# Performance work log

Measured on AMD Instinct MI355X. Metric: run time of the kernel, lower is better.

The kernel has to match this reference:

```python
import jax, jax.numpy as jnp
import numpy as np

TAU = 0.07
EPS = 1e-10


def setup_inputs() -> dict:
    key = jax.random.key(0)
    k1, k2 = jax.random.split(key)
    N, D = 8192, 128
    features = jax.random.normal(k1, (N, D), dtype=jnp.float32)
    alpha = jnp.float32(0.5)  # cosine-similarity threshold in (-1, 1)
    return {"features": features, "alpha": alpha}


def reference(features, alpha):
    # L2-normalize rows (torch F.normalize uses eps=1e-12 clamp on the norm)
    norm = jnp.maximum(jnp.linalg.norm(features, axis=1, keepdims=True), 1e-12)
    f = features / norm
    sim = f @ f.T  # [N, N]

    n = f.shape[0]
    not_eye = ~jnp.eye(n, dtype=bool)
    pos_mask = (sim >= alpha) & not_eye
    neg_mask = (sim < alpha) & not_eye

    e = jnp.exp(sim / TAU)  # [N, N], computed once and reused for both masks
    numerator = jnp.sum(jnp.where(pos_mask, e, 0.0), axis=1) + EPS
    denominator = numerator + jnp.sum(jnp.where(neg_mask, e, 0.0), axis=1) + EPS
    loss = -jnp.log(numerator / denominator)
    return loss.mean()
```

## Files before the change

### kernel.cpp

```cpp
#include <hip/hip_runtime.h>

#define N_ROWS 8192
#define BM 128
#define SEG 512
#define TILE 64
#define NTILE (SEG / TILE)
#define NSEG (N_ROWS / SEG)
#define NPART NSEG
#define KEXP 20.60992915f

typedef __attribute__((ext_vector_type(8))) short short8;
typedef __attribute__((ext_vector_type(4))) float f32x4;

__device__ __forceinline__ void gload_lds16(const void* g, void* l) {
  __builtin_amdgcn_global_load_lds(
      (const __attribute__((address_space(1))) void*)g,
      (__attribute__((address_space(3))) void*)l, 16, 0, 0);
}

__device__ __forceinline__ unsigned short f2bf(float x) {
  unsigned int u = __float_as_uint(x);
  unsigned int r = (u + 0x7fffu + ((u >> 16) & 1u)) >> 16;
  return (unsigned short)r;
}

__device__ __forceinline__ float fast_exp2(float x) {
  float r;
  asm("v_exp_f32 %0, %1" : "=v"(r) : "v"(x));
  return r;
}

__global__ __launch_bounds__(256) void knorm(const float* __restrict__ feat,
                                             unsigned int* __restrict__ fnA,
                                             unsigned int* __restrict__ fnB) {
  const int wid = threadIdx.x >> 6;
  const int lane = threadIdx.x & 63;
  const int row = blockIdx.x * 4 + wid;
  const float2 v = *(const float2*)(feat + (size_t)row * 128 + lane * 2);
  float s = v.x * v.x + v.y * v.y;
#pragma unroll
  for (int m = 1; m < 64; m <<= 1) s += __shfl_xor(s, m);
  const float inv = 1.0f / fmaxf(sqrtf(s), 1e-12f);
  const float x = v.x * inv, y = v.y * inv;
  const int cc = lane >> 2;
  const int idx = ((row >> 4) << 10) + ((cc >> 2) << 8) + ((cc & 3) << 6) +
                  ((row & 15) << 2) + (lane & 3);
  fnB[idx] = (unsigned int)f2bf(x) | ((unsigned int)f2bf(y) << 16);
  fnA[idx] = (unsigned int)f2bf(x * KEXP) | ((unsigned int)f2bf(y * KEXP) << 16);
}

__global__ __launch_bounds__(256, 4) void ksim(const unsigned int* __restrict__ fnA,
                                               const unsigned int* __restrict__ fnB,
                                               const float* __restrict__ alphap,
                                               float* __restrict__ posP,
                                               float* __restrict__ totP) {
  __shared__ __align__(16) char smem[32768];
  const int tid = threadIdx.x;
  const int lane = tid & 63;
  const int wid = tid >> 6;
  const int r0 = blockIdx.x * BM;
  const int c0 = blockIdx.y * SEG;
  const float alphaK = alphap[0] * KEXP;

  const char* __restrict__ FA = (const char*)fnA;
  const char* __restrict__ FB = (const char*)fnB;

  short8 aR[2][4];
  {
    const int G0 = (r0 + wid * 32) >> 4;
#pragma unroll
    for (int m = 0; m < 2; m++)
#pragma unroll
      for (int ks = 0; ks < 4; ks++)
        aR[m][ks] = *(const short8*)(FA + (size_t)(G0 + m) * 4096 + ks * 1024 + lane * 16);
  }

  {
    const char* g = FB + (size_t)(c0 >> 4) * 4096 + wid * 4096 + lane * 16;
    char* l = smem + wid * 4096;
#pragma unroll
    for (int s = 0; s < 4; s++) gload_lds16(g + s * 1024, l + s * 1024);
  }
  __syncthreads();

  float pp[2][4] = {{0.f}}, tp[2][4] = {{0.f}};
  int cur = 0;

#pragma unroll 1
  for (int it = 0; it < NTILE; ++it) {
    if (it + 1 < NTILE) {
      const char* g = FB + (size_t)((c0 >> 4) + (it + 1) * 4) * 4096 + wid * 4096 + lane * 16;
      char* l = smem + (cur ^ 1) * 16384 + wid * 4096;
#pragma unroll
      for (int s = 0; s < 4; s++) gload_lds16(g + s * 1024, l + s * 1024);
    }

    f32x4 acc[2][4];
#pragma unroll
    for (int m = 0; m < 2; m++)
#pragma unroll
      for (int n = 0; n < 4; n++) acc[m][n] = (f32x4){0.f, 0.f, 0.f, 0.f};

    const char* Bb = smem + cur * 16384;
#pragma unroll
    for (int ks = 0; ks < 4; ks++) {
      const short8 b0 = *(const short8*)(Bb + 0 * 4096 + ks * 1024 + lane * 16);
      const short8 b1 = *(const short8*)(Bb + 1 * 4096 + ks * 1024 + lane * 16);
      const short8 b2 = *(const short8*)(Bb + 2 * 4096 + ks * 1024 + lane * 16);
      const short8 b3 = *(const short8*)(Bb + 3 * 4096 + ks * 1024 + lane * 16);
#pragma unroll
      for (int m = 0; m < 2; m++) {
        acc[m][0] = __builtin_amdgcn_mfma_f32_16x16x32_bf16(aR[m][ks], b0, acc[m][0], 0, 0, 0);
        acc[m][1] = __builtin_amdgcn_mfma_f32_16x16x32_bf16(aR[m][ks], b1, acc[m][1], 0, 0, 0);
        acc[m][2] = __builtin_amdgcn_mfma_f32_16x16x32_bf16(aR[m][ks], b2, acc[m][2], 0, 0, 0);
        acc[m][3] = __builtin_amdgcn_mfma_f32_16x16x32_bf16(aR[m][ks], b3, acc[m][3], 0, 0, 0);
      }
    }

    const int cb = c0 + it * TILE;
#pragma unroll
    for (int m = 0; m < 2; m++) {
      const int grb = r0 + wid * 32 + m * 16;
#pragma unroll
      for (int n = 0; n < 4; n++) {
        const int gcb = cb + n * 16;
        const f32x4 a = acc[m][n];
        if (grb == gcb) {
          const int gr0 = (lane >> 4) << 2;
          const int gcl = lane & 15;
#pragma unroll
          for (int r = 0; r < 4; r++) {
            const float e = fast_exp2(a[r]);
            const float ev = (gr0 + r == gcl) ? 0.0f : e;
            tp[m][r] += ev;
            pp[m][r] += (a[r] >= alphaK) ? ev : 0.0f;
          }
        } else {
#pragma unroll
          for (int r = 0; r < 4; r++) {
            const float e = fast_exp2(a[r]);
            tp[m][r] += e;
            pp[m][r] += (a[r] >= alphaK) ? e : 0.0f;
          }
        }
      }
    }
    __syncthreads();
    cur ^= 1;
  }

#pragma unroll
  for (int m = 0; m < 2; m++)
#pragma unroll
    for (int r = 0; r < 4; r++) {
      float p = pp[m][r], t = tp[m][r];
#pragma unroll
      for (int msk = 1; msk < 16; msk <<= 1) {
        p += __shfl_xor(p, msk);
        t += __shfl_xor(t, msk);
      }
      if ((lane & 15) == 0) {
        const int row = r0 + wid * 32 + m * 16 + ((lane >> 4) << 2) + r;
        posP[blockIdx.y * N_ROWS + row] = p;
        totP[blockIdx.y * N_ROWS + row] = t;
      }
    }
}

__global__ __launch_bounds__(128) void kred1(const float* __restrict__ posP,
                                             const float* __restrict__ totP,
                                             float* __restrict__ bp) {
  const int t = threadIdx.x;
  const int row = blockIdx.x * 128 + t;
  float pos = 0.f, tot = 0.f;
#pragma unroll
  for (int c = 0; c < NPART; c++) {
    pos += posP[c * N_ROWS + row];
    tot += totP[c * N_ROWS + row];
  }
  float term = __logf(tot + 2e-10f) - __logf(pos + 1e-10f);
#pragma unroll
  for (int m = 1; m < 64; m <<= 1) term += __shfl_xor(term, m);
  __shared__ float s2[2];
  if ((t & 63) == 0) s2[t >> 6] = term;
  __syncthreads();
  if (t == 0) bp[blockIdx.x] = s2[0] + s2[1];
}

__global__ void kred2(const float* __restrict__ bp, float* __restrict__ out) {
  const int l = threadIdx.x;
  float v = bp[l];
#pragma unroll
  for (int m = 1; m < 64; m <<= 1) v += __shfl_xor(v, m);
  if (l == 0) out[0] = v * (1.0f / 8192.0f);
}

extern "C" void kernel_launch(void* const* d_in, const int* in_sizes, int n_in,
                              void* d_out, int out_size, void* d_ws, size_t ws_size,
                              hipStream_t stream) {
  const float* feat = (const float*)d_in[0];
  const float* alphap = (const float*)d_in[1];
  char* ws = (char*)d_ws;
  unsigned int* fnA = (unsigned int*)ws;
  unsigned int* fnB = (unsigned int*)(ws + (2u << 20));
  float* posP = (float*)(ws + (4u << 20));
  float* totP = (float*)(ws + (5u << 20));
  float* bp = (float*)(ws + (6u << 20));
  float* out = (float*)d_out;

  knorm<<<dim3(N_ROWS / 4), dim3(256), 0, stream>>>(feat, fnA, fnB);
  ksim<<<dim3(N_ROWS / BM, NSEG), dim3(256), 0, stream>>>(fnA, fnB, alphap, posP, totP);
  kred1<<<dim3(N_ROWS / 128), dim3(128), 0, stream>>>(posP, totP, bp);
  kred2<<<dim3(1), dim3(64), 0, stream>>>(bp, out);
}
```

Before: 37.42 us.

## Load B tiles directly from global memory instead of LDS double-buffering

Removes the LDS staging buffer and the double-buffered global_load_lds prefetch of the B tiles. Each wave now reads its B fragments straight from global memory, relying on L1/L2 caching because all four waves read the same tile. The per-tile __syncthreads barriers go away and the loop is unrolled by two so loads can be issued ahead. The risk is more global and L2 traffic and exposed load latency, since the explicit prefetch is gone.

```diff
diff --git a/kernel.cpp b/kernel.cpp
--- a/kernel.cpp
+++ b/kernel.cpp
@@ -11,12 +11,6 @@
 
 typedef __attribute__((ext_vector_type(8))) short short8;
 typedef __attribute__((ext_vector_type(4))) float f32x4;
-
-__device__ __forceinline__ void gload_lds16(const void* g, void* l) {
-  __builtin_amdgcn_global_load_lds(
-      (const __attribute__((address_space(1))) void*)g,
-      (__attribute__((address_space(3))) void*)l, 16, 0, 0);
-}
 
 __device__ __forceinline__ unsigned short f2bf(float x) {
   unsigned int u = __float_as_uint(x);
@@ -54,7 +48,6 @@
                                                const float* __restrict__ alphap,
                                                float* __restrict__ posP,
                                                float* __restrict__ totP) {
-  __shared__ __align__(16) char smem[32768];
   const int tid = threadIdx.x;
   const int lane = tid & 63;
   const int wid = tid >> 6;
@@ -75,25 +68,11 @@
         aR[m][ks] = *(const short8*)(FA + (size_t)(G0 + m) * 4096 + ks * 1024 + lane * 16);
   }
 
-  {
-    const char* g = FB + (size_t)(c0 >> 4) * 4096 + wid * 4096 + lane * 16;
-    char* l = smem + wid * 4096;
-#pragma unroll
-    for (int s = 0; s < 4; s++) gload_lds16(g + s * 1024, l + s * 1024);
-  }
-  __syncthreads();
+  float pp[2][4] = {{0.f}}, tp[2][4] = {{0.f}};
 
-  float pp[2][4] = {{0.f}}, tp[2][4] = {{0.f}};
-  int cur = 0;
-
-#pragma unroll 1
+#pragma unroll 2
   for (int it = 0; it < NTILE; ++it) {
-    if (it + 1 < NTILE) {
-      const char* g = FB + (size_t)((c0 >> 4) + (it + 1) * 4) * 4096 + wid * 4096 + lane * 16;
-      char* l = smem + (cur ^ 1) * 16384 + wid * 4096;
-#pragma unroll
-      for (int s = 0; s < 4; s++) gload_lds16(g + s * 1024, l + s * 1024);
-    }
+    const char* Bb = FB + (size_t)((c0 >> 4) + it * 4) * 4096 + lane * 16;
 
     f32x4 acc[2][4];
 #pragma unroll
@@ -101,13 +80,12 @@
 #pragma unroll
       for (int n = 0; n < 4; n++) acc[m][n] = (f32x4){0.f, 0.f, 0.f, 0.f};
 
-    const char* Bb = smem + cur * 16384;
 #pragma unroll
     for (int ks = 0; ks < 4; ks++) {
-      const short8 b0 = *(const short8*)(Bb + 0 * 4096 + ks * 1024 + lane * 16);
-      const short8 b1 = *(const short8*)(Bb + 1 * 4096 + ks * 1024 + lane * 16);
-      const short8 b2 = *(const short8*)(Bb + 2 * 4096 + ks * 1024 + lane * 16);
-      const short8 b3 = *(const short8*)(Bb + 3 * 4096 + ks * 1024 + lane * 16);
+      const short8 b0 = *(const short8*)(Bb + 0 * 4096 + ks * 1024);
+      const short8 b1 = *(const short8*)(Bb + 1 * 4096 + ks * 1024);
+      const short8 b2 = *(const short8*)(Bb + 2 * 4096 + ks * 1024);
+      const short8 b3 = *(const short8*)(Bb + 3 * 4096 + ks * 1024);
 #pragma unroll
       for (int m = 0; m < 2; m++) {
         acc[m][0] = __builtin_amdgcn_mfma_f32_16x16x32_bf16(aR[m][ks], b0, acc[m][0], 0, 0, 0);
@@ -145,8 +123,6 @@
         }
       }
     }
-    __syncthreads();
-    cur ^= 1;
   }
 
 #pragma unroll
```

Measured after the change: 96.95 us. +159.1%, slower.
